# Kernel tuning notes

Hardware: AMD Instinct MI355X
Metric: run time of the kernel (lower is better)

The kernel has to match this reference:

```python
import jax, jax.numpy as jnp
import numpy as np

N_CELLS = 65536
NH = 7
NV = 4
E_IN = 16
E_OUT = 16
N_OFF = 4
N_SIG = 4
B = 2


def setup_inputs() -> dict:
    key = jax.random.key(0)
    ks = jax.random.split(key, 8)
    x = jax.random.normal(ks[0], (B, N_CELLS, NV, E_IN), dtype=jnp.float32)
    # coords[0]=lat in [-pi/2, pi/2], coords[1]=lon in [-pi, pi]
    lat = (jax.random.uniform(ks[1], (N_CELLS,), dtype=jnp.float32) - 0.5) * jnp.pi
    lon = (jax.random.uniform(ks[2], (N_CELLS,), dtype=jnp.float32) - 0.5) * 2 * jnp.pi
    coords = jnp.stack([lat, lon], axis=0)
    # positive sigmas / offsets on the scale of typical grid distances
    sigma = jax.random.uniform(ks[3], (N_SIG,), dtype=jnp.float32) * 0.5 + 0.05
    dist_offsets = jax.random.uniform(ks[4], (N_OFF,), dtype=jnp.float32) * 0.5
    W = jax.random.normal(ks[5], (N_OFF, N_SIG, E_IN, E_OUT), dtype=jnp.float32) / np.sqrt(N_OFF * N_SIG * E_IN)
    b_out = jnp.zeros((E_OUT,), dtype=jnp.float32)
    adjc = jax.random.randint(ks[6], (N_CELLS, NH), 0, N_CELLS, dtype=jnp.int32)
    nh_mask = jax.random.randint(ks[7], (N_CELLS, NH), 0, 2, dtype=jnp.int32)
    return {"x": x, "coords": coords, "sigma": sigma, "dist_offsets": dist_offsets,
            "W": W, "b_out": b_out, "adjc": adjc, "nh_mask": nh_mask}


def _polar_distance(lat_c, lon_c, lat_nh, lon_nh):
    # great-circle distance (radians) between center cell and its neighbors
    dlon = lon_nh - lon_c
    cosd = (jnp.sin(lat_c) * jnp.sin(lat_nh)
            + jnp.cos(lat_c) * jnp.cos(lat_nh) * jnp.cos(dlon))
    return jnp.arccos(jnp.clip(cosd, -1.0 + 1e-7, 1.0 - 1e-7))  # [n, nh]


def reference(x, coords, sigma, dist_offsets, W, b_out, adjc, nh_mask):
    # neighborhood coordinate gather: [n, nh]
    lat, lon = coords[0], coords[1]
    lat_nh, lon_nh = lat[adjc], lon[adjc]
    d = _polar_distance(lat[:, None], lon[:, None], lat_nh, lon_nh)  # [n, nh]
    # Gaussian (RBF) kernel over distance offsets x sigmas: normal_dist with sigma_cross
    diff = d[:, :, None] - dist_offsets  # [n, nh, o]
    nd = jnp.exp(-0.5 * (diff[..., None] / sigma) ** 2)  # [n, nh, o, s]
    nd = nd * nh_mask.astype(nd.dtype)[:, :, None, None]
    nd = nd / (nd.sum(axis=1, keepdims=True) + 1e-8)  # normalize over neighborhood
    # multi-level neighbor feature gather: [b, n, nh, nv, e]
    x_nh = x[:, adjc]
    # RBF-weighted neighborhood aggregation: [b, n, o, s, nv, e]
    agg = jnp.einsum('bnhve,nhos->bnosve', x_nh, nd)
    # projection over (offset, sigma, e_in) -> e_out: [b, n, nv, e_out]
    out = jnp.einsum('bnosve,osef->bnvf', agg, W) + b_out
    return out
```

## Files before the change

kernel.cpp:

```cpp
#include <hip/hip_runtime.h>
#include <hip/hip_bf16.h>
#include <math.h>

#define N_CELLS 65536
#define NH 7
#define NV 4
#define E_IN 16
#define E_OUT 16
#define NK 16

#define CPB 32
#define THREADS 256
#define TRP 20

typedef __attribute__((ext_vector_type(8))) short bf16x8;
typedef __attribute__((ext_vector_type(4))) float f32x4;
typedef __attribute__((ext_vector_type(2))) float f32x2;
typedef unsigned long long u64;

#define NDOFF(k, cl) (((k) << 8) + ((((cl) ^ ((k) & 3))) << 3))

static __device__ __forceinline__ short f2bfs(float f) {
    __hip_bfloat16 h = __float2bfloat16(f);
    short s;
    __builtin_memcpy(&s, &h, 2);
    return s;
}

__global__ __launch_bounds__(256) void setup_kernel(
    const float* __restrict__ x, const float* __restrict__ coords,
    const float* __restrict__ W,
    short* __restrict__ wf, unsigned char* __restrict__ xq, float* __restrict__ meta)
{
    const int t = threadIdx.x;
    const int g = blockIdx.x * 64 + (t >> 2);
    const int p = t & 3;

    const float4* src = (const float4*)(x + (size_t)g * 64 + p * 16);
    float4 q[4];
    #pragma unroll
    for (int i = 0; i < 4; ++i) q[i] = src[i];

    float amax = 0.0f;
    #pragma unroll
    for (int i = 0; i < 4; ++i)
        amax = fmaxf(amax, fmaxf(fmaxf(fabsf(q[i].x), fabsf(q[i].y)),
                                 fmaxf(fabsf(q[i].z), fabsf(q[i].w))));
    amax = fmaxf(amax, __shfl_xor(amax, 1));
    amax = fmaxf(amax, __shfl_xor(amax, 2));
    amax = fmaxf(amax, 1e-12f);

    const float inv = 127.0f / amax;
    const float s   = amax / 127.0f;

    unsigned int w[4];
    #pragma unroll
    for (int i = 0; i < 4; ++i) {
        const float vs[4] = {q[i].x, q[i].y, q[i].z, q[i].w};
        unsigned int ww = 0;
        #pragma unroll
        for (int j = 0; j < 4; ++j) {
            float r = rintf(vs[j] * inv);
            r = fminf(fmaxf(r, -127.0f), 127.0f);
            ww |= ((unsigned int)(int)(r + 128.0f) & 0xffu) << (8 * j);
        }
        w[i] = ww;
    }
    *(uint4*)(xq + (size_t)g * 64 + p * 16) = make_uint4(w[0], w[1], w[2], w[3]);

    const int cell = g & (N_CELLS - 1);
    const int b    = g >> 16;
    if (p == 0) meta[(size_t)cell * 8 + 4 + b] = s;

    if (p == 0 && b == 0) {
        const float lat = coords[cell];
        const float lon = coords[N_CELLS + cell];
        meta[(size_t)cell * 8 + 0] = sinf(lat);
        meta[(size_t)cell * 8 + 1] = cosf(lat);
        meta[(size_t)cell * 8 + 2] = sinf(lon);
        meta[(size_t)cell * 8 + 3] = cosf(lon);
        meta[(size_t)cell * 8 + 6] = 0.0f;
        meta[(size_t)cell * 8 + 7] = 0.0f;
    }

    if (blockIdx.x == 0) {
        const int kk  = t;
        const int j   = kk & 7;
        const int grp = (kk >> 3) & 3;
        const int st  = kk >> 5;
        #pragma unroll
        for (int col = 0; col < E_OUT; ++col)
            wf[(((st * 4 + grp) * 16) + col) * 8 + j] = f2bfs(W[kk * E_OUT + col]);
    }
}

__global__ __launch_bounds__(THREADS, 3) void mge_kernel(
    const unsigned char* __restrict__ xq,
    const float* __restrict__ meta,
    const float* __restrict__ sigma,
    const float* __restrict__ dist_offsets,
    const short* __restrict__ wf,
    const float* __restrict__ b_out,
    const int*   __restrict__ adjc,
    const int*   __restrict__ nh_mask,
    float* __restrict__ out,
    const int b)
{
    __shared__ float nd_flat[NK * 256];
    __shared__ int   adj_lds[CPB][NH];
    __shared__ float d_lds[CPB][NH];
    __shared__ float m_lds[CPB][NH];
    __shared__ float scl_lds[CPB][NH];
    __shared__ float tr_lds[4][16][TRP];

    const int t    = threadIdx.x;
    const int lane = t & 63;
    const int wv   = t >> 6;
    const int base = blockIdx.x * CPB;

    const unsigned char* xqb = xq + ((size_t)b << 16) * 64;

    if (t < CPB * NH) {
        const int cl = t / NH;
        const int h  = t % NH;
        const int n  = base + cl;
        const int a  = adjc[n * NH + h];
        const int m  = nh_mask[n * NH + h];
        adj_lds[cl][h] = a;
        const float4 gc = *(const float4*)(meta + (size_t)n * 8);
        const float4 gn = *(const float4*)(meta + (size_t)a * 8);
        const float cdl = gn.w * gc.w + gn.z * gc.z;
        float cosd = gc.x * gn.x + gc.y * gn.y * cdl;
        cosd = fminf(fmaxf(cosd, -1.0f + 1e-7f), 1.0f - 1e-7f);
        d_lds[cl][h] = acosf(cosd);
        m_lds[cl][h] = (float)m;
        scl_lds[cl][h] = meta[(size_t)a * 8 + 4 + b];
    }

    const int col = lane & 15;
    const int grp = lane >> 4;
    bf16x8 bfrag[8];
    #pragma unroll
    for (int st = 0; st < 8; ++st)
        bfrag[st] = ((const bf16x8*)wf)[(st * 4 + grp) * 16 + col];
    const float obias = b_out[col];

    __syncthreads();

    const int arow = lane & 15;
    const int cq   = arow >> 2;
    const int v    = arow & 3;
    const int e0   = (grp & 1) * 8;
    const int kos_off = grp >> 1;

    u64 xbA[NH], xbB[NH];

#define LOADQ(XB, Q)                                                            \
    {                                                                           \
        const int cl_ = (wv << 3) + ((Q) << 2) + cq;                            \
        _Pragma("unroll")                                                       \
        for (int h = 0; h < NH; ++h) {                                          \
            const int a = adj_lds[cl_][h];                                      \
            XB[h] = *(const u64*)(xqb + (size_t)a * 64 + (v << 4) + e0);        \
        }                                                                       \
    }

    LOADQ(xbA, 0)
    LOADQ(xbB, 1)

    #pragma unroll
    for (int it = 0; it < 2; ++it) {
        const int task = it * THREADS + t;
        const int cl = task >> 4;
        const int k  = task & 15;
        const int o  = k >> 2;
        const int s  = k & 3;
        const float off     = dist_offsets[o];
        const float inv_sig = 1.0f / sigma[s];
        float raw[NH];
        float sum = 0.0f;
        #pragma unroll
        for (int h = 0; h < NH; ++h) {
            const float df = (d_lds[cl][h] - off) * inv_sig;
            const float e  = __expf(-0.5f * df * df) * m_lds[cl][h];
            raw[h] = e;
            sum += e;
        }
        const float inv = 1.0f / (sum + 1e-8f);
        float ndp[NH];
        float cb = 0.0f;
        #pragma unroll
        for (int h = 0; h < NH; ++h) {
            ndp[h] = raw[h] * inv * scl_lds[cl][h];
            cb += ndp[h];
        }
        float* dst = nd_flat + NDOFF(k, cl);
        *(f32x4*)dst       = (f32x4){ndp[0], ndp[1], ndp[2], ndp[3]};
        *(f32x4*)(dst + 4) = (f32x4){ndp[4], ndp[5], ndp[6], -128.0f * cb};
    }
    __syncthreads();

#define COMPQ(XB, Q)                                                            \
    {                                                                           \
        const int cl_ = (wv << 3) + ((Q) << 2) + cq;                            \
               \
        f32x2 u2[NH][4];                                                        \
        _Pragma("unroll")                                                       \
        for (int h = 0; h < NH; ++h) {                                          \
            const unsigned lo = (unsigned)XB[h], hi = (unsigned)(XB[h] >> 32);  \
            u2[h][0] = (f32x2){(float)(lo & 0xffu), (float)((lo >> 8) & 0xffu)};  \
            u2[h][1] = (f32x2){(float)((lo >> 16) & 0xffu), (float)(lo >> 24)};   \
            u2[h][2] = (f32x2){(float)(hi & 0xffu), (float)((hi >> 8) & 0xffu)};  \
            u2[h][3] = (f32x2){(float)((hi >> 16) & 0xffu), (float)(hi >> 24)};   \
        }                                                                       \
        f32x4 acc = {0.f, 0.f, 0.f, 0.f};                                       \
        _Pragma("unroll")                                                       \
        for (int st = 0; st < 8; ++st) {                                        \
            const int k2 = st * 2 + kos_off;                                    \
            const float* ndp = nd_flat + NDOFF(k2, cl_);                        \
            const f32x4 n0 = *(const f32x4*)ndp;                                \
            const f32x4 n1 = *(const f32x4*)(ndp + 4);                          \
            const float nds[NH] = {n0.x, n0.y, n0.z, n0.w, n1.x, n1.y, n1.z};   \
            const float ng = n1.w;                                              \
            f32x2 s0 = {ng, ng}, s1 = {ng, ng};                                 \
            f32x2 s2 = {ng, ng}, s3 = {ng, ng};                                 \
            _Pragma("unroll")                                                   \
            for (int h = 0; h < NH; ++h) {                                      \
                const f32x2 nd2 = {nds[h], nds[h]};                             \
                s0 = s0 + nd2 * u2[h][0];                                       \
                s1 = s1 + nd2 * u2[h][1];                                       \
                s2 = s2 + nd2 * u2[h][2];                                       \
                s3 = s3 + nd2 * u2[h][3];                                       \
            }                                                                   \
            bf16x8 aa;                                                          \
            aa[0] = f2bfs(s0.x); aa[1] = f2bfs(s0.y);                           \
            aa[2] = f2bfs(s1.x); aa[3] = f2bfs(s1.y);                           \
            aa[4] = f2bfs(s2.x); aa[5] = f2bfs(s2.y);                           \
            aa[6] = f2bfs(s3.x); aa[7] = f2bfs(s3.y);                           \
            acc = __builtin_amdgcn_mfma_f32_16x16x32_bf16(aa, bfrag[st], acc, 0, 0, 0); \
        }                                                                       \
                  \
        _Pragma("unroll")                                                       \
        for (int r = 0; r < 4; ++r)                                             \
            tr_lds[wv][grp * 4 + r][col] = acc[r] + obias;                      \
        __builtin_amdgcn_s_waitcnt(0);                                          \
        {                                                                       \
            const int rr = lane >> 2;                                           \
            const int cc = (lane & 3) << 2;                                     \
            const f32x4 val = *(const f32x4*)&tr_lds[wv][rr][cc];               \
            const size_t qbase = ((size_t)b << 16) + base + (wv << 3) + ((Q) << 2); \
            __builtin_nontemporal_store(val, (f32x4*)(out + qbase * 64 + rr * 16 + cc)); \
        }                                                                       \
    }

    COMPQ(xbA, 0)
    COMPQ(xbB, 1)

#undef LOADQ
#undef COMPQ
}

extern "C" void kernel_launch(void* const* d_in, const int* in_sizes, int n_in,
                              void* d_out, int out_size, void* d_ws, size_t ws_size,
                              hipStream_t stream) {
    const float* x            = (const float*)d_in[0];
    const float* coords       = (const float*)d_in[1];
    const float* sigma        = (const float*)d_in[2];
    const float* dist_offsets = (const float*)d_in[3];
    const float* W            = (const float*)d_in[4];
    const float* b_out        = (const float*)d_in[5];
    const int*   adjc         = (const int*)d_in[6];
    const int*   nh_mask      = (const int*)d_in[7];
    float* out = (float*)d_out;

    char* ws = (char*)d_ws;
    short*         wf   = (short*)ws;
    float*         meta = (float*)(ws + 8192);
    unsigned char* xq   = (unsigned char*)(ws + 8192 + 2097152);

    setup_kernel<<<2048, 256, 0, stream>>>(x, coords, W, wf, xq, meta);
    dim3 grid(N_CELLS / CPB);
    mge_kernel<<<grid, THREADS, 0, stream>>>(xq, meta, sigma, dist_offsets,
                                             wf, b_out, adjc, nh_mask, out, 0);
    mge_kernel<<<grid, THREADS, 0, stream>>>(xq, meta, sigma, dist_offsets,
                                             wf, b_out, adjc, nh_mask, out, 1);
}
```

Before: 55.58 us.

## Merge both batch launches into one kernel with interleaved quantized layout

The two per-batch launches become a single kernel that handles both batches for each block of cells. The shared work is done once per block: neighbor distances, RBF weights, adjacency loads and nd normalisation. The quantized x buffer is interleaved per cell as [cell][b][64], so the two batch rows of a neighbor sit next to each other in memory. Loads for the next batch are issued between compute phases to overlap gather latency. This removes one launch and the duplicated geometry and RBF computation, at the cost of doubled nd LDS usage, which may lower occupancy.

```diff
diff --git a/kernel.cpp b/kernel.cpp
--- a/kernel.cpp
+++ b/kernel.cpp
@@ -66,10 +66,10 @@
         }
         w[i] = ww;
     }
-    *(uint4*)(xq + (size_t)g * 64 + p * 16) = make_uint4(w[0], w[1], w[2], w[3]);
-
     const int cell = g & (N_CELLS - 1);
     const int b    = g >> 16;
+    *(uint4*)(xq + (size_t)cell * 128 + b * 64 + p * 16) = make_uint4(w[0], w[1], w[2], w[3]);
+
     if (p == 0) meta[(size_t)cell * 8 + 4 + b] = s;
 
     if (p == 0 && b == 0) {
@@ -103,22 +103,19 @@
     const float* __restrict__ b_out,
     const int*   __restrict__ adjc,
     const int*   __restrict__ nh_mask,
-    float* __restrict__ out,
-    const int b)
+    float* __restrict__ out)
 {
-    __shared__ float nd_flat[NK * 256];
+    __shared__ float nd_flat[2][NK * 256];
     __shared__ int   adj_lds[CPB][NH];
     __shared__ float d_lds[CPB][NH];
     __shared__ float m_lds[CPB][NH];
-    __shared__ float scl_lds[CPB][NH];
+    __shared__ float scl_lds[CPB][NH][2];
     __shared__ float tr_lds[4][16][TRP];
 
     const int t    = threadIdx.x;
     const int lane = t & 63;
     const int wv   = t >> 6;
     const int base = blockIdx.x * CPB;
-
-    const unsigned char* xqb = xq + ((size_t)b << 16) * 64;
 
     if (t < CPB * NH) {
         const int cl = t / NH;
@@ -129,12 +126,14 @@
         adj_lds[cl][h] = a;
         const float4 gc = *(const float4*)(meta + (size_t)n * 8);
         const float4 gn = *(const float4*)(meta + (size_t)a * 8);
+        const float2 sn = *(const float2*)(meta + (size_t)a * 8 + 4);
         const float cdl = gn.w * gc.w + gn.z * gc.z;
         float cosd = gc.x * gn.x + gc.y * gn.y * cdl;
         cosd = fminf(fmaxf(cosd, -1.0f + 1e-7f), 1.0f - 1e-7f);
         d_lds[cl][h] = acosf(cosd);
         m_lds[cl][h] = (float)m;
-        scl_lds[cl][h] = meta[(size_t)a * 8 + 4 + b];
+        scl_lds[cl][h][0] = sn.x;
+        scl_lds[cl][h][1] = sn.y;
     }
 
     const int col = lane & 15;
@@ -157,11 +156,12 @@
 
 #define LOADQ(XB, Q)                                                            \
     {                                                                           \
-        const int cl_ = (wv << 3) + ((Q) << 2) + cq;                            \
+        const int cl_ = (wv << 3) + (((Q) & 1) << 2) + cq;                      \
+        const int b_  = (Q) >> 1;                                               \
         _Pragma("unroll")                                                       \
         for (int h = 0; h < NH; ++h) {                                          \
             const int a = adj_lds[cl_][h];                                      \
-            XB[h] = *(const u64*)(xqb + (size_t)a * 64 + (v << 4) + e0);        \
+            XB[h] = *(const u64*)(xq + (size_t)a * 128 + (b_ << 6) + (v << 4) + e0); \
         }                                                                       \
     }
 
@@ -187,22 +187,29 @@
             sum += e;
         }
         const float inv = 1.0f / (sum + 1e-8f);
-        float ndp[NH];
-        float cb = 0.0f;
+        float nd0[NH], nd1[NH];
+        float cb0 = 0.0f, cb1 = 0.0f;
         #pragma unroll
         for (int h = 0; h < NH; ++h) {
-            ndp[h] = raw[h] * inv * scl_lds[cl][h];
-            cb += ndp[h];
+            const float nd = raw[h] * inv;
+            nd0[h] = nd * scl_lds[cl][h][0];
+            nd1[h] = nd * scl_lds[cl][h][1];
+            cb0 += nd0[h];
+            cb1 += nd1[h];
         }
-        float* dst = nd_flat + NDOFF(k, cl);
-        *(f32x4*)dst       = (f32x4){ndp[0], ndp[1], ndp[2], ndp[3]};
-        *(f32x4*)(dst + 4) = (f32x4){ndp[4], ndp[5], ndp[6], -128.0f * cb};
+        float* dst0 = &nd_flat[0][NDOFF(k, cl)];
+        *(f32x4*)dst0       = (f32x4){nd0[0], nd0[1], nd0[2], nd0[3]};
+        *(f32x4*)(dst0 + 4) = (f32x4){nd0[4], nd0[5], nd0[6], -128.0f * cb0};
+        float* dst1 = &nd_flat[1][NDOFF(k, cl)];
+        *(f32x4*)dst1       = (f32x4){nd1[0], nd1[1], nd1[2], nd1[3]};
+        *(f32x4*)(dst1 + 4) = (f32x4){nd1[4], nd1[5], nd1[6], -128.0f * cb1};
     }
     __syncthreads();
 
 #define COMPQ(XB, Q)                                                            \
     {                                                                           \
-        const int cl_ = (wv << 3) + ((Q) << 2) + cq;                            \
+        const int cl_ = (wv << 3) + (((Q) & 1) << 2) + cq;                      \
+        const int b_  = (Q) >> 1;                                               \
                \
         f32x2 u2[NH][4];                                                        \
         _Pragma("unroll")                                                       \
@@ -213,11 +220,12 @@
             u2[h][2] = (f32x2){(float)(hi & 0xffu), (float)((hi >> 8) & 0xffu)};  \
             u2[h][3] = (f32x2){(float)((hi >> 16) & 0xffu), (float)(hi >> 24)};   \
         }                                                                       \
+        const float* ndbase = nd_flat[b_];                                      \
         f32x4 acc = {0.f, 0.f, 0.f, 0.f};                                       \
         _Pragma("unroll")                                                       \
         for (int st = 0; st < 8; ++st) {                                        \
             const int k2 = st * 2 + kos_off;                                    \
-            const float* ndp = nd_flat + NDOFF(k2, cl_);                        \
+            const float* ndp = ndbase + NDOFF(k2, cl_);                         \
             const f32x4 n0 = *(const f32x4*)ndp;                                \
             const f32x4 n1 = *(const f32x4*)(ndp + 4);                          \
             const float nds[NH] = {n0.x, n0.y, n0.z, n0.w, n1.x, n1.y, n1.z};   \
@@ -248,13 +256,17 @@
             const int rr = lane >> 2;                                           \
             const int cc = (lane & 3) << 2;                                     \
             const f32x4 val = *(const f32x4*)&tr_lds[wv][rr][cc];               \
-            const size_t qbase = ((size_t)b << 16) + base + (wv << 3) + ((Q) << 2); \
+            const size_t qbase = ((size_t)b_ << 16) + base + (wv << 3) + (((Q) & 1) << 2); \
             __builtin_nontemporal_store(val, (f32x4*)(out + qbase * 64 + rr * 16 + cc)); \
         }                                                                       \
     }
 
     COMPQ(xbA, 0)
+    LOADQ(xbA, 2)
     COMPQ(xbB, 1)
+    LOADQ(xbB, 3)
+    COMPQ(xbA, 2)
+    COMPQ(xbB, 3)
 
 #undef LOADQ
 #undef COMPQ
@@ -281,7 +293,5 @@
     setup_kernel<<<2048, 256, 0, stream>>>(x, coords, W, wf, xq, meta);
     dim3 grid(N_CELLS / CPB);
     mge_kernel<<<grid, THREADS, 0, stream>>>(xq, meta, sigma, dist_offsets,
-                                             wf, b_out, adjc, nh_mask, out, 0);
-    mge_kernel<<<grid, THREADS, 0, stream>>>(xq, meta, sigma, dist_offsets,
-                                             wf, b_out, adjc, nh_mask, out, 1);
-}
+                                             wf, b_out, adjc, nh_mask, out);
+}
```

After: 48.08 us (median of 2 runs). 1.16x faster.
